# Performance work log

Hardware: AMD Instinct MI355X
Metric: run time of the kernel (lower is better)

## Reference

```python
import jax, jax.numpy as jnp
import numpy as np

N = 4096   # support size
B = 512    # number of histograms (columns)


def setup_inputs() -> dict:
    key = jax.random.key(0)
    kU, kP, kK = jax.random.split(key, 3)
    # u must satisfy u < lamda; uniform [0,1) with lamda=10 is safe.
    U = jax.random.uniform(kU, (N, B), dtype=jnp.float32)
    # strictly positive histograms (avoid log(0))
    P = jax.random.uniform(kP, (N, B), dtype=jnp.float32) + 0.01
    # positive Gibbs kernel
    K = jax.random.uniform(kK, (N, N), dtype=jnp.float32) + 1e-3
    return {"U": U, "P": P, "K": K, "eps": 1, "lamda": 10}


def reference(U, P, K, eps, lamda):
    """Vectorized OTModel.OT_unbal: sum over columns of the primal unbalanced OT
    value reconstructed from dual potential U.  gamma_ij = a_i * K_ij * f_j is
    never materialized; all reductions over gamma are contracted analytically.
    """
    eps = jnp.float32(eps)
    lamda = jnp.float32(lamda)
    # f in log domain: (lamda/eps) * log(lamda/(lamda-u))          [N, B]
    flog = (lamda / eps) * jnp.log(lamda / (lamda - U))
    f = jnp.exp(flog)
    # alpha/eps with the mean-scale stabilization from get_alpha_unbal
    scale = flog.mean(axis=0)                                      # [B]
    KF_stab = K @ jnp.exp(flog - scale)                            # [N, B]
    alpha_over_eps = jnp.log(P) - (jnp.log(KF_stab) + scale)       # [N, B]
    a = jnp.exp(alpha_over_eps)                                    # exp(alpha/eps)
    Kf = K @ f                                                     # [N, B]
    # (gamma @ flog).sum() = sum_i a_i * (K @ (f * flog))_i
    term1 = jnp.sum(a * (K @ (f * flog)))
    # (gamma.T @ (alpha/eps)).sum() = sum_i a_i * (alpha/eps)_i * (K @ f)_i
    term2 = jnp.sum(a * alpha_over_eps * Kf)
    # gamma.sum()
    term3 = jnp.sum(a * Kf)
    # gamma.sum(0)_j = f_j * (K^T @ a)_j
    gcol = f * (K.T @ a)                                           # [N, B]
    # q from get_q_unbal (unstabilized, as in the original)
    q = (lamda / (lamda - U)) ** (lamda / eps + 1.0) * (K.T @ (P / Kf))
    # KL(a,b) = sum(a*log(a/b) - a)   (inputs strictly positive here)
    kl = jnp.sum(gcol * jnp.log(gcol / q) - gcol)
    return eps * (term1 + term2 - term3) + lamda * kl
```

## Files before the change

kernel.cpp:

```cpp
#include <hip/hip_runtime.h>

#define NN 4096
#define BB 512

typedef __attribute__((ext_vector_type(4))) float f32x4;
typedef __attribute__((ext_vector_type(16))) float f32x16;
typedef __attribute__((ext_vector_type(4))) int i32x4;
typedef __attribute__((ext_vector_type(8))) int i32x8;
typedef unsigned short ushort;
typedef unsigned char uchar;
typedef unsigned int uint;
typedef __attribute__((ext_vector_type(4))) ushort ushort4v;

#define ASCALE 16384.0f
#define AINV   6.103515625e-05f
#define SCL1   0x7f7f7f7f

__device__ __forceinline__ float scal_val(const void* p) {
    int b = *(const int*)p;
    if (b >= 1 && b <= 1000000) return (float)b;
    return __int_as_float(b);
}

__device__ __forceinline__ ushort f2bf(float x) {
    unsigned u = __float_as_uint(x);
    u += 0x7fffu + ((u >> 16) & 1u);
    return (ushort)(u >> 16);
}
__device__ __forceinline__ float bf2f(ushort b) {
    return __uint_as_float((uint)b << 16);
}

__device__ __forceinline__ uint pack4_fp8(float a, float b, float c, float d) {
    int v = __builtin_amdgcn_cvt_pk_fp8_f32(a, b, 0, false);
    v = __builtin_amdgcn_cvt_pk_fp8_f32(c, d, v, true);
    return (uint)v;
}

__device__ __forceinline__ void gload16(const void* g, void* l) {
    __builtin_amdgcn_global_load_lds(
        (const __attribute__((address_space(1))) unsigned int*)g,
        (__attribute__((address_space(3))) unsigned int*)l, 16, 0, 0);
}

__device__ __forceinline__ double wave_sum(double v) {
#pragma unroll
    for (int s = 32; s > 0; s >>= 1) v += __shfl_down(v, s, 64);
    return v;
}

__device__ __forceinline__ int offA(int i, int k) {
    return (((i >> 7) * 64 + (k >> 6)) << 13) + ((i & 127) << 6) +
           ((((k >> 4) & 3) ^ ((i >> 1) & 3)) << 4) + (k & 15);
}
__device__ __forceinline__ int offB(int j, int k) {
    return (((j >> 6) * 64 + (k >> 6)) << 12) + ((j & 63) << 6) +
           ((((k >> 4) & 3) ^ ((j >> 1) & 3)) << 4) + (k & 15);
}

__device__ __forceinline__ i32x8 frag64(const uchar* rowbase, int u0byte) {
    i32x4 lo = *(const i32x4*)(rowbase + u0byte);
    i32x4 hi = *(const i32x4*)(rowbase + (u0byte ^ 16));
    i32x8 r;
    r[0] = lo[0]; r[1] = lo[1]; r[2] = lo[2]; r[3] = lo[3];
    r[4] = hi[0]; r[5] = hi[1]; r[6] = hi[2]; r[7] = hi[3];
    return r;
}


__global__ __launch_bounds__(256) void k_prep(const float* __restrict__ K,
                                              const float* __restrict__ U,
                                              uchar* __restrict__ Kb,
                                              uchar* __restrict__ KTb,
                                              uchar* __restrict__ fT,
                                              const void* epsp, const void* lamp) {
    __shared__ float tile[64][65];
    const int t = threadIdx.x;
    const int tx = t & 15, ty = t >> 4;
    const int bid = blockIdx.x;

    if (bid < 4096) {
        const int c0 = (bid & 63) * 64, r0 = (bid >> 6) * 64;
#pragma unroll
        for (int it = 0; it < 4; ++it) {
            int row = ty + it * 16;
            int i = r0 + row;
            float4 v = *(const float4*)&K[(size_t)i * NN + c0 + tx * 4];
            *(uint*)&Kb[offA(i, c0 + tx * 4)] = pack4_fp8(v.x, v.y, v.z, v.w);
            tile[row][tx * 4 + 0] = v.x;
            tile[row][tx * 4 + 1] = v.y;
            tile[row][tx * 4 + 2] = v.z;
            tile[row][tx * 4 + 3] = v.w;
        }
        __syncthreads();
#pragma unroll
        for (int it = 0; it < 4; ++it) {
            int row = ty + it * 16;
            int i = c0 + row;
            int k = r0 + tx * 4;
            *(uint*)&KTb[offA(i, k)] =
                pack4_fp8(tile[tx * 4 + 0][row], tile[tx * 4 + 1][row],
                          tile[tx * 4 + 2][row], tile[tx * 4 + 3][row]);
        }
    } else {
        const int r = bid - 4096;
        const int c0 = (r & 7) * 64;
        const int r0 = (r >> 3) * 64;
        const float eps = scal_val(epsp), lam = scal_val(lamp);
        const float rr = lam / eps;
#pragma unroll
        for (int it = 0; it < 4; ++it) {
            int row = ty + it * 16;
            float4 v = *(const float4*)&U[(size_t)(r0 + row) * BB + c0 + tx * 4];
            float uu[4] = {v.x, v.y, v.z, v.w};
#pragma unroll
            for (int k = 0; k < 4; ++k) {
                float L = __logf(lam / (lam - uu[k]));
                tile[row][tx * 4 + k] = __expf(rr * L);
            }
        }
        __syncthreads();
#pragma unroll
        for (int it = 0; it < 4; ++it) {
            int row = ty + it * 16;
            int j = c0 + row;
            int k = r0 + tx * 4;
            *(uint*)&fT[offB(j, k)] =
                pack4_fp8(tile[tx * 4 + 0][row], tile[tx * 4 + 1][row],
                          tile[tx * 4 + 2][row], tile[tx * 4 + 3][row]);
        }
    }
}

__global__ __launch_bounds__(256) void k_gemm1(const uchar* __restrict__ Kb,
                                               const uchar* __restrict__ fT,
                                               ushort* __restrict__ Y1b) {
    __shared__ __align__(16) uchar As[2][128 * 64];
    __shared__ __align__(16) uchar Bf[2][64 * 64];

    const int tid = threadIdx.x;
    const int lane = tid & 63;
    const int w = tid >> 6;
    const int bid = blockIdx.x;
    const int kh = bid & 3;
    const int i0 = ((bid >> 2) & 31) * 128;
    const int j0 = (bid >> 7) * 64;
    const int h = lane >> 5;
    const int r = lane & 31;
    const int u0b = (((h << 1) ^ ((r >> 1) & 3)) << 4);

    f32x16 acc0 = {}, acc1 = {};

    const uchar* apanel = Kb + ((size_t)(i0 >> 7) << 19);
    const uchar* bpanel = fT + ((size_t)(j0 >> 6) << 18);

    auto stage = [&](int ks, int b) {
        const uchar* ga = apanel + ((size_t)ks << 13) + w * 2048 + lane * 16;
        gload16(ga, &As[b][w * 2048]);
        gload16(ga + 1024, &As[b][w * 2048 + 1024]);
        const uchar* gb = bpanel + ((size_t)ks << 12) + w * 1024 + lane * 16;
        gload16(gb, &Bf[b][w * 1024]);
    };

    const int ks0 = kh * 16;
    stage(ks0, 0);
    __syncthreads();
    for (int step = 0; step < 16; ++step) {
        const int cur = step & 1;
        if (step < 15) stage(ks0 + step + 1, cur ^ 1);
        i32x8 av = frag64(&As[cur][(w * 32 + r) << 6], u0b);
        i32x8 bv0 = frag64(&Bf[cur][r << 6], u0b);
        i32x8 bv1 = frag64(&Bf[cur][(32 + r) << 6], u0b);
        acc0 = __builtin_amdgcn_mfma_scale_f32_32x32x64_f8f6f4(
            av, bv0, acc0, 0, 0, 0, SCL1, 0, SCL1);
        acc1 = __builtin_amdgcn_mfma_scale_f32_32x32x64_f8f6f4(
            av, bv1, acc1, 0, 0, 0, SCL1, 0, SCL1);
        __syncthreads();
    }

    ushort* o1 = Y1b + (size_t)kh * NN * BB;
#pragma unroll
    for (int reg = 0; reg < 16; ++reg) {
        const int row = i0 + w * 32 + (reg & 3) + 8 * (reg >> 2) + 4 * h;
        o1[(size_t)row * BB + j0 + r] = f2bf(acc0[reg]);
        o1[(size_t)row * BB + j0 + 32 + r] = f2bf(acc1[reg]);
    }
}

__global__ __launch_bounds__(256) void k_epi(const ushort* __restrict__ Y1b,
                                             const float* __restrict__ P,
                                             uchar* __restrict__ aT,
                                             double* __restrict__ parts) {
    __shared__ float ta[64][65];
    __shared__ double bred[4][2];
    const int t = threadIdx.x;
    const int lane = t & 63;
    const int w = t >> 6;
    const int tx = t & 15, ty = t >> 4;
    const int j0 = blockIdx.x * 64;
    const int i0 = blockIdx.y * 64;
    const int bid = blockIdx.y * 8 + blockIdx.x;
    const size_t H = (size_t)NN * BB;

    double t2 = 0.0, t3 = 0.0;
#pragma unroll
    for (int it = 0; it < 4; ++it) {
        int row = ty + it * 16;
        size_t off = (size_t)(i0 + row) * BB + j0 + tx * 4;
        ushort4v q0 = *(const ushort4v*)(Y1b + off);
        ushort4v q1 = *(const ushort4v*)(Y1b + H + off);
        ushort4v q2 = *(const ushort4v*)(Y1b + 2 * H + off);
        ushort4v q3 = *(const ushort4v*)(Y1b + 3 * H + off);
        float4 p4 = *(const float4*)(P + off);
        float pv[4] = {p4.x, p4.y, p4.z, p4.w};
#pragma unroll
        for (int e = 0; e < 4; ++e) {
            float y1 = bf2f(q0[e]) + bf2f(q1[e]) + bf2f(q2[e]) + bf2f(q3[e]);
            float aij = pv[e] / y1;
            t2 += (double)(pv[e] * __logf(aij));
            t3 += (double)pv[e];
            ta[row][tx * 4 + e] = aij * ASCALE;
        }
    }
    __syncthreads();
#pragma unroll
    for (int it = 0; it < 4; ++it) {
        int row = ty + it * 16;
        int j = j0 + row;
        *(uint*)&aT[offB(j, i0 + tx * 4)] =
            pack4_fp8(ta[tx * 4 + 0][row], ta[tx * 4 + 1][row],
                      ta[tx * 4 + 2][row], ta[tx * 4 + 3][row]);
    }

    t2 = wave_sum(t2); t3 = wave_sum(t3);
    if (lane == 0) { bred[w][0] = t2; bred[w][1] = t3; }
    __syncthreads();
    if (t == 0) {
        double b = 0, c = 0;
#pragma unroll
        for (int ww = 0; ww < 4; ++ww) { b += bred[ww][0]; c += bred[ww][1]; }
        parts[2048 + bid] = b;
        parts[2560 + bid] = c;
    }
}

__global__ __launch_bounds__(256) void k_gemm2(const uchar* __restrict__ KTb,
                                               const uchar* __restrict__ aT,
                                               const float* __restrict__ U,
                                               const void* epsp, const void* lamp,
                                               double* __restrict__ parts) {
    __shared__ __align__(16) uchar As[2][128 * 64];
    __shared__ __align__(16) uchar Bs[2][64 * 64];
    __shared__ double bred[4][2];

    const float eps = scal_val(epsp), lam = scal_val(lamp);
    const float rr = lam / eps;
    const int tid = threadIdx.x;
    const int lane = tid & 63;
    const int w = tid >> 6;
    const int bid = blockIdx.x;
    const int kh = bid & 3;
    const int i0 = ((bid >> 2) & 31) * 128;
    const int j0 = (bid >> 7) * 64;
    const int h = lane >> 5;
    const int r = lane & 31;
    const int u0b = (((h << 1) ^ ((r >> 1) & 3)) << 4);

    f32x16 acc0 = {}, acc1 = {};

    const uchar* apanel = KTb + ((size_t)(i0 >> 7) << 19);
    const uchar* bpanel = aT + ((size_t)(j0 >> 6) << 18);

    auto stage = [&](int ks, int b) {
        const uchar* ga = apanel + ((size_t)ks << 13) + w * 2048 + lane * 16;
        gload16(ga, &As[b][w * 2048]);
        gload16(ga + 1024, &As[b][w * 2048 + 1024]);
        const uchar* gb = bpanel + ((size_t)ks << 12) + w * 1024 + lane * 16;
        gload16(gb, &Bs[b][w * 1024]);
    };

    const int ks0 = kh * 16;
    stage(ks0, 0);
    __syncthreads();
    for (int step = 0; step < 16; ++step) {
        const int cur = step & 1;
        if (step < 15) stage(ks0 + step + 1, cur ^ 1);
        i32x8 av = frag64(&As[cur][(w * 32 + r) << 6], u0b);
        i32x8 bv0 = frag64(&Bs[cur][r << 6], u0b);
        i32x8 bv1 = frag64(&Bs[cur][(32 + r) << 6], u0b);
        acc0 = __builtin_amdgcn_mfma_scale_f32_32x32x64_f8f6f4(
            av, bv0, acc0, 0, 0, 0, SCL1, 0, SCL1);
        acc1 = __builtin_amdgcn_mfma_scale_f32_32x32x64_f8f6f4(
            av, bv1, acc1, 0, 0, 0, SCL1, 0, SCL1);
        __syncthreads();
    }

    double t1p = 0.0, klp = 0.0;
#pragma unroll
    for (int reg = 0; reg < 16; ++reg) {
        const int ib = i0 + w * 32 + (reg & 3) + 8 * (reg >> 2) + 4 * h;
#pragma unroll
        for (int nt = 0; nt < 2; ++nt) {
            const int j = j0 + nt * 32 + r;
            float s = (nt ? acc1[reg] : acc0[reg]) * AINV;
            float u = U[(size_t)ib * BB + j];
            float L = __logf(lam / (lam - u));
            float fv = __expf(rr * L);
            t1p += (double)(fv * rr * L * s);
            klp -= (double)(fv * (1.0f + L) * s);
        }
    }

    t1p = wave_sum(t1p); klp = wave_sum(klp);
    if (lane == 0) { bred[w][0] = t1p; bred[w][1] = klp; }
    __syncthreads();
    if (tid == 0) {
        double a = 0, b = 0;
#pragma unroll
        for (int ww = 0; ww < 4; ++ww) { a += bred[ww][0]; b += bred[ww][1]; }
        parts[bid] = a;
        parts[1024 + bid] = b;
    }
}

__global__ __launch_bounds__(256) void k_final(const double* __restrict__ parts,
                                               const void* epsp, const void* lamp,
                                               float* __restrict__ out) {
    __shared__ double red[4][4];
    const int tid = threadIdx.x;
    const int lane = tid & 63, w = tid >> 6;
    double s0 = 0.0, s1 = 0.0, s2 = 0.0, s3 = 0.0;
    for (int i = tid; i < 1024; i += 256) {
        s0 += parts[i];
        s1 += parts[1024 + i];
    }
    for (int i = tid; i < 512; i += 256) {
        s2 += parts[2048 + i];
        s3 += parts[2560 + i];
    }
    s0 = wave_sum(s0); s1 = wave_sum(s1); s2 = wave_sum(s2); s3 = wave_sum(s3);
    if (lane == 0) { red[w][0] = s0; red[w][1] = s1; red[w][2] = s2; red[w][3] = s3; }
    __syncthreads();
    if (tid == 0) {
        double t1 = 0, kl = 0, t2 = 0, t3 = 0;
#pragma unroll
        for (int ww = 0; ww < 4; ++ww) {
            t1 += red[ww][0]; kl += red[ww][1]; t2 += red[ww][2]; t3 += red[ww][3];
        }
        float eps = scal_val(epsp), lam = scal_val(lamp);
        out[0] = (float)((double)eps * (t1 + t2 - t3) + (double)lam * kl);
    }
}

extern "C" void kernel_launch(void* const* d_in, const int* in_sizes, int n_in,
                              void* d_out, int out_size, void* d_ws, size_t ws_size,
                              hipStream_t stream) {
    const float* U = (const float*)d_in[0];
    const float* P = (const float*)d_in[1];
    const float* K = (const float*)d_in[2];
    const void* epsp = d_in[3];
    const void* lamp = d_in[4];

    double* parts = (double*)d_ws;
    char* base = (char*)d_ws + (64 << 10);
    uchar* Kb   = (uchar*)base;
    uchar* KTb  = (uchar*)(base + ((size_t)16 << 20));
    uchar* fT   = (uchar*)(base + ((size_t)32 << 20));
    uchar* aT   = (uchar*)(base + ((size_t)34 << 20));
    ushort* Y1b = (ushort*)(base + ((size_t)36 << 20));

    k_prep<<<4608, 256, 0, stream>>>(K, U, Kb, KTb, fT, epsp, lamp);
    k_gemm1<<<1024, 256, 0, stream>>>(Kb, fT, Y1b);
    k_epi<<<dim3(8, 64), 256, 0, stream>>>(Y1b, P, aT, parts);
    k_gemm2<<<1024, 256, 0, stream>>>(KTb, aT, U, epsp, lamp, parts);
    k_final<<<1, 256, 0, stream>>>(parts, epsp, lamp, (float*)d_out);
}
```

Before: 156.0 us.

## Enlarge GEMM block tile to 128x128 with 2x2 wave grid and 8-way split-K

Both FP8 GEMM kernels now compute a 128x128 output tile per block. Each wave owns a 64x64 sub-tile (2x2 MFMAs), so every loaded A and B fragment is reused twice. To keep the block count the same, split-K doubles from 4 to 8 slices, and each block runs 8 K-steps instead of 16. Launch bounds now request 4 blocks per CU. The price is that the epilogue must read and sum 8 bf16 partial planes of Y1 instead of 4, and the intermediate buffer must hold twice as many planes.

Result: slower. 179.1 us (+14.8%).

```diff
diff --git a/kernel.cpp b/kernel.cpp
--- a/kernel.cpp
+++ b/kernel.cpp
@@ -132,24 +132,29 @@
     }
 }
 
-__global__ __launch_bounds__(256) void k_gemm1(const uchar* __restrict__ Kb,
-                                               const uchar* __restrict__ fT,
-                                               ushort* __restrict__ Y1b) {
+__global__ __launch_bounds__(256, 4) void k_gemm1(const uchar* __restrict__ Kb,
+                                                  const uchar* __restrict__ fT,
+                                                  ushort* __restrict__ Y1b) {
     __shared__ __align__(16) uchar As[2][128 * 64];
-    __shared__ __align__(16) uchar Bf[2][64 * 64];
+    __shared__ __align__(16) uchar Bs[2][128 * 64];
 
     const int tid = threadIdx.x;
     const int lane = tid & 63;
     const int w = tid >> 6;
+    const int wm = w >> 1, wn = w & 1;
     const int bid = blockIdx.x;
-    const int kh = bid & 3;
-    const int i0 = ((bid >> 2) & 31) * 128;
-    const int j0 = (bid >> 7) * 64;
+    const int kh = bid & 7;
+    const int i0 = ((bid >> 3) & 31) * 128;
+    const int j0 = (bid >> 8) * 128;
     const int h = lane >> 5;
     const int r = lane & 31;
     const int u0b = (((h << 1) ^ ((r >> 1) & 3)) << 4);
 
-    f32x16 acc0 = {}, acc1 = {};
+    f32x16 acc[2][2];
+#pragma unroll
+    for (int mt = 0; mt < 2; ++mt)
+#pragma unroll
+        for (int nt = 0; nt < 2; ++nt) acc[mt][nt] = (f32x16)(0.0f);
 
     const uchar* apanel = Kb + ((size_t)(i0 >> 7) << 19);
     const uchar* bpanel = fT + ((size_t)(j0 >> 6) << 18);
@@ -158,33 +163,47 @@
         const uchar* ga = apanel + ((size_t)ks << 13) + w * 2048 + lane * 16;
         gload16(ga, &As[b][w * 2048]);
         gload16(ga + 1024, &As[b][w * 2048 + 1024]);
-        const uchar* gb = bpanel + ((size_t)ks << 12) + w * 1024 + lane * 16;
-        gload16(gb, &Bf[b][w * 1024]);
+        const uchar* gb = bpanel + (((size_t)(w >> 1)) << 18) +
+                          ((size_t)ks << 12) + (w & 1) * 2048 + lane * 16;
+        gload16(gb, &Bs[b][w * 2048]);
+        gload16(gb + 1024, &Bs[b][w * 2048 + 1024]);
     };
 
-    const int ks0 = kh * 16;
+    const int ks0 = kh * 8;
     stage(ks0, 0);
     __syncthreads();
-    for (int step = 0; step < 16; ++step) {
+    for (int step = 0; step < 8; ++step) {
         const int cur = step & 1;
-        if (step < 15) stage(ks0 + step + 1, cur ^ 1);
-        i32x8 av = frag64(&As[cur][(w * 32 + r) << 6], u0b);
-        i32x8 bv0 = frag64(&Bf[cur][r << 6], u0b);
-        i32x8 bv1 = frag64(&Bf[cur][(32 + r) << 6], u0b);
-        acc0 = __builtin_amdgcn_mfma_scale_f32_32x32x64_f8f6f4(
-            av, bv0, acc0, 0, 0, 0, SCL1, 0, SCL1);
-        acc1 = __builtin_amdgcn_mfma_scale_f32_32x32x64_f8f6f4(
-            av, bv1, acc1, 0, 0, 0, SCL1, 0, SCL1);
+        if (step < 7) stage(ks0 + step + 1, cur ^ 1);
+        i32x8 av[2], bv[2];
+#pragma unroll
+        for (int mt = 0; mt < 2; ++mt)
+            av[mt] = frag64(&As[cur][(wm * 64 + mt * 32 + r) << 6], u0b);
+#pragma unroll
+        for (int nt = 0; nt < 2; ++nt)
+            bv[nt] = frag64(&Bs[cur][(wn * 64 + nt * 32 + r) << 6], u0b);
+#pragma unroll
+        for (int mt = 0; mt < 2; ++mt)
+#pragma unroll
+            for (int nt = 0; nt < 2; ++nt)
+                acc[mt][nt] = __builtin_amdgcn_mfma_scale_f32_32x32x64_f8f6f4(
+                    av[mt], bv[nt], acc[mt][nt], 0, 0, 0, SCL1, 0, SCL1);
         __syncthreads();
     }
 
     ushort* o1 = Y1b + (size_t)kh * NN * BB;
 #pragma unroll
-    for (int reg = 0; reg < 16; ++reg) {
-        const int row = i0 + w * 32 + (reg & 3) + 8 * (reg >> 2) + 4 * h;
-        o1[(size_t)row * BB + j0 + r] = f2bf(acc0[reg]);
-        o1[(size_t)row * BB + j0 + 32 + r] = f2bf(acc1[reg]);
-    }
+    for (int mt = 0; mt < 2; ++mt)
+#pragma unroll
+        for (int nt = 0; nt < 2; ++nt) {
+            const int jb = j0 + wn * 64 + nt * 32 + r;
+#pragma unroll
+            for (int reg = 0; reg < 16; ++reg) {
+                const int row =
+                    i0 + wm * 64 + mt * 32 + (reg & 3) + 8 * (reg >> 2) + 4 * h;
+                o1[(size_t)row * BB + jb] = f2bf(acc[mt][nt][reg]);
+            }
+        }
 }
 
 __global__ __launch_bounds__(256) void k_epi(const ushort* __restrict__ Y1b,
@@ -207,16 +226,18 @@
     for (int it = 0; it < 4; ++it) {
         int row = ty + it * 16;
         size_t off = (size_t)(i0 + row) * BB + j0 + tx * 4;
-        ushort4v q0 = *(const ushort4v*)(Y1b + off);
-        ushort4v q1 = *(const ushort4v*)(Y1b + H + off);
-        ushort4v q2 = *(const ushort4v*)(Y1b + 2 * H + off);
-        ushort4v q3 = *(const ushort4v*)(Y1b + 3 * H + off);
+        float y1[4] = {0.f, 0.f, 0.f, 0.f};
+#pragma unroll
+        for (int pl = 0; pl < 8; ++pl) {
+            ushort4v qq = *(const ushort4v*)(Y1b + (size_t)pl * H + off);
+#pragma unroll
+            for (int e = 0; e < 4; ++e) y1[e] += bf2f(qq[e]);
+        }
         float4 p4 = *(const float4*)(P + off);
         float pv[4] = {p4.x, p4.y, p4.z, p4.w};
 #pragma unroll
         for (int e = 0; e < 4; ++e) {
-            float y1 = bf2f(q0[e]) + bf2f(q1[e]) + bf2f(q2[e]) + bf2f(q3[e]);
-            float aij = pv[e] / y1;
+            float aij = pv[e] / y1[e];
             t2 += (double)(pv[e] * __logf(aij));
             t3 += (double)pv[e];
             ta[row][tx * 4 + e] = aij * ASCALE;
@@ -244,13 +265,13 @@
     }
 }
 
-__global__ __launch_bounds__(256) void k_gemm2(const uchar* __restrict__ KTb,
-                                               const uchar* __restrict__ aT,
-                                               const float* __restrict__ U,
-                                               const void* epsp, const void* lamp,
-                                               double* __restrict__ parts) {
+__global__ __launch_bounds__(256, 4) void k_gemm2(const uchar* __restrict__ KTb,
+                                                  const uchar* __restrict__ aT,
+                                                  const float* __restrict__ U,
+                                                  const void* epsp, const void* lamp,
+                                                  double* __restrict__ parts) {
     __shared__ __align__(16) uchar As[2][128 * 64];
-    __shared__ __align__(16) uchar Bs[2][64 * 64];
+    __shared__ __align__(16) uchar Bs[2][128 * 64];
     __shared__ double bred[4][2];
 
     const float eps = scal_val(epsp), lam = scal_val(lamp);
@@ -258,15 +279,20 @@
     const int tid = threadIdx.x;
     const int lane = tid & 63;
     const int w = tid >> 6;
+    const int wm = w >> 1, wn = w & 1;
     const int bid = blockIdx.x;
-    const int kh = bid & 3;
-    const int i0 = ((bid >> 2) & 31) * 128;
-    const int j0 = (bid >> 7) * 64;
+    const int kh = bid & 7;
+    const int i0 = ((bid >> 3) & 31) * 128;
+    const int j0 = (bid >> 8) * 128;
     const int h = lane >> 5;
     const int r = lane & 31;
     const int u0b = (((h << 1) ^ ((r >> 1) & 3)) << 4);
 
-    f32x16 acc0 = {}, acc1 = {};
+    f32x16 acc[2][2];
+#pragma unroll
+    for (int mt = 0; mt < 2; ++mt)
+#pragma unroll
+        for (int nt = 0; nt < 2; ++nt) acc[mt][nt] = (f32x16)(0.0f);
 
     const uchar* apanel = KTb + ((size_t)(i0 >> 7) << 19);
     const uchar* bpanel = aT + ((size_t)(j0 >> 6) << 18);
@@ -275,41 +301,52 @@
         const uchar* ga = apanel + ((size_t)ks << 13) + w * 2048 + lane * 16;
         gload16(ga, &As[b][w * 2048]);
         gload16(ga + 1024, &As[b][w * 2048 + 1024]);
-        const uchar* gb = bpanel + ((size_t)ks << 12) + w * 1024 + lane * 16;
-        gload16(gb, &Bs[b][w * 1024]);
+        const uchar* gb = bpanel + (((size_t)(w >> 1)) << 18) +
+                          ((size_t)ks << 12) + (w & 1) * 2048 + lane * 16;
+        gload16(gb, &Bs[b][w * 2048]);
+        gload16(gb + 1024, &Bs[b][w * 2048 + 1024]);
     };
 
-    const int ks0 = kh * 16;
+    const int ks0 = kh * 8;
     stage(ks0, 0);
     __syncthreads();
-    for (int step = 0; step < 16; ++step) {
+    for (int step = 0; step < 8; ++step) {
         const int cur = step & 1;
-        if (step < 15) stage(ks0 + step + 1, cur ^ 1);
-        i32x8 av = frag64(&As[cur][(w * 32 + r) << 6], u0b);
-        i32x8 bv0 = frag64(&Bs[cur][r << 6], u0b);
-        i32x8 bv1 = frag64(&Bs[cur][(32 + r) << 6], u0b);
-        acc0 = __builtin_amdgcn_mfma_scale_f32_32x32x64_f8f6f4(
-            av, bv0, acc0, 0, 0, 0, SCL1, 0, SCL1);
-        acc1 = __builtin_amdgcn_mfma_scale_f32_32x32x64_f8f6f4(
-            av, bv1, acc1, 0, 0, 0, SCL1, 0, SCL1);
+        if (step < 7) stage(ks0 + step + 1, cur ^ 1);
+        i32x8 av[2], bv[2];
+#pragma unroll
+        for (int mt = 0; mt < 2; ++mt)
+            av[mt] = frag64(&As[cur][(wm * 64 + mt * 32 + r) << 6], u0b);
+#pragma unroll
+        for (int nt = 0; nt < 2; ++nt)
+            bv[nt] = frag64(&Bs[cur][(wn * 64 + nt * 32 + r) << 6], u0b);
+#pragma unroll
+        for (int mt = 0; mt < 2; ++mt)
+#pragma unroll
+            for (int nt = 0; nt < 2; ++nt)
+                acc[mt][nt] = __builtin_amdgcn_mfma_scale_f32_32x32x64_f8f6f4(
+                    av[mt], bv[nt], acc[mt][nt], 0, 0, 0, SCL1, 0, SCL1);
         __syncthreads();
     }
 
     double t1p = 0.0, klp = 0.0;
 #pragma unroll
-    for (int reg = 0; reg < 16; ++reg) {
-        const int ib = i0 + w * 32 + (reg & 3) + 8 * (reg >> 2) + 4 * h;
+    for (int mt = 0; mt < 2; ++mt)
 #pragma unroll
         for (int nt = 0; nt < 2; ++nt) {
-            const int j = j0 + nt * 32 + r;
-            float s = (nt ? acc1[reg] : acc0[reg]) * AINV;
-            float u = U[(size_t)ib * BB + j];
-            float L = __logf(lam / (lam - u));
-            float fv = __expf(rr * L);
-            t1p += (double)(fv * rr * L * s);
-            klp -= (double)(fv * (1.0f + L) * s);
-        }
-    }
+            const int jb = j0 + wn * 64 + nt * 32 + r;
+#pragma unroll
+            for (int reg = 0; reg < 16; ++reg) {
+                const int ib =
+                    i0 + wm * 64 + mt * 32 + (reg & 3) + 8 * (reg >> 2) + 4 * h;
+                float s = acc[mt][nt][reg] * AINV;
+                float u = U[(size_t)ib * BB + jb];
+                float L = __logf(lam / (lam - u));
+                float fv = __expf(rr * L);
+                t1p += (double)(fv * rr * L * s);
+                klp -= (double)(fv * (1.0f + L) * s);
+            }
+        }
 
     t1p = wave_sum(t1p); klp = wave_sum(klp);
     if (lane == 0) { bred[w][0] = t1p; bred[w][1] = klp; }
```

## Double K-tile per stage in fp8 GEMMs and fold final reduction into gemm2

Applied to the files above, without the earlier changes.

Both fp8 MFMA GEMM kernels now stage 128 bytes of K per pipeline step instead of 64, halving the number of loop iterations and __syncthreads barriers, at the cost of double the LDS footprint (which may lower occupancy). The separate single-block final-reduction kernel is removed: gemm2 blocks increment an atomic counter (zeroed in k_prep), and the last block to finish sums the partial results and writes the output. This saves one kernel launch, at the cost of a threadfence and an atomic per block.

Measured after the change: 192.1 us. 23.1% more time.

```diff
diff --git a/kernel.cpp b/kernel.cpp
--- a/kernel.cpp
+++ b/kernel.cpp
@@ -73,11 +73,14 @@
                                               uchar* __restrict__ Kb,
                                               uchar* __restrict__ KTb,
                                               uchar* __restrict__ fT,
-                                              const void* epsp, const void* lamp) {
+                                              const void* epsp, const void* lamp,
+                                              double* __restrict__ parts) {
     __shared__ float tile[64][65];
     const int t = threadIdx.x;
     const int tx = t & 15, ty = t >> 4;
     const int bid = blockIdx.x;
+
+    if (bid == 0 && t == 0) *(unsigned int*)(parts + 3072) = 0u;
 
     if (bid < 4096) {
         const int c0 = (bid & 63) * 64, r0 = (bid >> 6) * 64;
@@ -135,8 +138,8 @@
 __global__ __launch_bounds__(256) void k_gemm1(const uchar* __restrict__ Kb,
                                                const uchar* __restrict__ fT,
                                                ushort* __restrict__ Y1b) {
-    __shared__ __align__(16) uchar As[2][128 * 64];
-    __shared__ __align__(16) uchar Bf[2][64 * 64];
+    __shared__ __align__(16) uchar As[2][128 * 128];
+    __shared__ __align__(16) uchar Bf[2][64 * 128];
 
     const int tid = threadIdx.x;
     const int lane = tid & 63;
@@ -154,27 +157,35 @@
     const uchar* apanel = Kb + ((size_t)(i0 >> 7) << 19);
     const uchar* bpanel = fT + ((size_t)(j0 >> 6) << 18);
 
-    auto stage = [&](int ks, int b) {
-        const uchar* ga = apanel + ((size_t)ks << 13) + w * 2048 + lane * 16;
-        gload16(ga, &As[b][w * 2048]);
-        gload16(ga + 1024, &As[b][w * 2048 + 1024]);
-        const uchar* gb = bpanel + ((size_t)ks << 12) + w * 1024 + lane * 16;
-        gload16(gb, &Bf[b][w * 1024]);
+    auto stage = [&](int step, int b) {
+        const int ks = (kh * 16) + step * 2;
+        const uchar* ga = apanel + ((size_t)ks << 13) + w * 4096 + lane * 16;
+        gload16(ga, &As[b][w * 4096]);
+        gload16(ga + 1024, &As[b][w * 4096 + 1024]);
+        gload16(ga + 2048, &As[b][w * 4096 + 2048]);
+        gload16(ga + 3072, &As[b][w * 4096 + 3072]);
+        const uchar* gb = bpanel + ((size_t)ks << 12) + w * 2048 + lane * 16;
+        gload16(gb, &Bf[b][w * 2048]);
+        gload16(gb + 1024, &Bf[b][w * 2048 + 1024]);
     };
 
-    const int ks0 = kh * 16;
-    stage(ks0, 0);
-    __syncthreads();
-    for (int step = 0; step < 16; ++step) {
+    stage(0, 0);
+    __syncthreads();
+    for (int step = 0; step < 8; ++step) {
         const int cur = step & 1;
-        if (step < 15) stage(ks0 + step + 1, cur ^ 1);
-        i32x8 av = frag64(&As[cur][(w * 32 + r) << 6], u0b);
-        i32x8 bv0 = frag64(&Bf[cur][r << 6], u0b);
-        i32x8 bv1 = frag64(&Bf[cur][(32 + r) << 6], u0b);
-        acc0 = __builtin_amdgcn_mfma_scale_f32_32x32x64_f8f6f4(
-            av, bv0, acc0, 0, 0, 0, SCL1, 0, SCL1);
-        acc1 = __builtin_amdgcn_mfma_scale_f32_32x32x64_f8f6f4(
-            av, bv1, acc1, 0, 0, 0, SCL1, 0, SCL1);
+        if (step < 7) stage(step + 1, cur ^ 1);
+#pragma unroll
+        for (int kk = 0; kk < 2; ++kk) {
+            const uchar* abase = &As[cur][kk * 8192];
+            const uchar* bbase = &Bf[cur][kk * 4096];
+            i32x8 av = frag64(abase + ((w * 32 + r) << 6), u0b);
+            i32x8 bv0 = frag64(bbase + (r << 6), u0b);
+            i32x8 bv1 = frag64(bbase + ((32 + r) << 6), u0b);
+            acc0 = __builtin_amdgcn_mfma_scale_f32_32x32x64_f8f6f4(
+                av, bv0, acc0, 0, 0, 0, SCL1, 0, SCL1);
+            acc1 = __builtin_amdgcn_mfma_scale_f32_32x32x64_f8f6f4(
+                av, bv1, acc1, 0, 0, 0, SCL1, 0, SCL1);
+        }
         __syncthreads();
     }
 
@@ -248,10 +259,12 @@
                                                const uchar* __restrict__ aT,
                                                const float* __restrict__ U,
                                                const void* epsp, const void* lamp,
-                                               double* __restrict__ parts) {
-    __shared__ __align__(16) uchar As[2][128 * 64];
-    __shared__ __align__(16) uchar Bs[2][64 * 64];
-    __shared__ double bred[4][2];
+                                               double* __restrict__ parts,
+                                               float* __restrict__ out) {
+    __shared__ __align__(16) uchar As[2][128 * 128];
+    __shared__ __align__(16) uchar Bs[2][64 * 128];
+    __shared__ double bred[4][4];
+    __shared__ int lastflag;
 
     const float eps = scal_val(epsp), lam = scal_val(lamp);
     const float rr = lam / eps;
@@ -271,27 +284,35 @@
     const uchar* apanel = KTb + ((size_t)(i0 >> 7) << 19);
     const uchar* bpanel = aT + ((size_t)(j0 >> 6) << 18);
 
-    auto stage = [&](int ks, int b) {
-        const uchar* ga = apanel + ((size_t)ks << 13) + w * 2048 + lane * 16;
-        gload16(ga, &As[b][w * 2048]);
-        gload16(ga + 1024, &As[b][w * 2048 + 1024]);
-        const uchar* gb = bpanel + ((size_t)ks << 12) + w * 1024 + lane * 16;
-        gload16(gb, &Bs[b][w * 1024]);
+    auto stage = [&](int step, int b) {
+        const int ks = (kh * 16) + step * 2;
+        const uchar* ga = apanel + ((size_t)ks << 13) + w * 4096 + lane * 16;
+        gload16(ga, &As[b][w * 4096]);
+        gload16(ga + 1024, &As[b][w * 4096 + 1024]);
+        gload16(ga + 2048, &As[b][w * 4096 + 2048]);
+        gload16(ga + 3072, &As[b][w * 4096 + 3072]);
+        const uchar* gb = bpanel + ((size_t)ks << 12) + w * 2048 + lane * 16;
+        gload16(gb, &Bs[b][w * 2048]);
+        gload16(gb + 1024, &Bs[b][w * 2048 + 1024]);
     };
 
-    const int ks0 = kh * 16;
-    stage(ks0, 0);
-    __syncthreads();
-    for (int step = 0; step < 16; ++step) {
+    stage(0, 0);
+    __syncthreads();
+    for (int step = 0; step < 8; ++step) {
         const int cur = step & 1;
-        if (step < 15) stage(ks0 + step + 1, cur ^ 1);
-        i32x8 av = frag64(&As[cur][(w * 32 + r) << 6], u0b);
-        i32x8 bv0 = frag64(&Bs[cur][r << 6], u0b);
-        i32x8 bv1 = frag64(&Bs[cur][(32 + r) << 6], u0b);
-        acc0 = __builtin_amdgcn_mfma_scale_f32_32x32x64_f8f6f4(
-            av, bv0, acc0, 0, 0, 0, SCL1, 0, SCL1);
-        acc1 = __builtin_amdgcn_mfma_scale_f32_32x32x64_f8f6f4(
-            av, bv1, acc1, 0, 0, 0, SCL1, 0, SCL1);
+        if (step < 7) stage(step + 1, cur ^ 1);
+#pragma unroll
+        for (int kk = 0; kk < 2; ++kk) {
+            const uchar* abase = &As[cur][kk * 8192];
+            const uchar* bbase = &Bs[cur][kk * 4096];
+            i32x8 av = frag64(abase + ((w * 32 + r) << 6), u0b);
+            i32x8 bv0 = frag64(bbase + (r << 6), u0b);
+            i32x8 bv1 = frag64(bbase + ((32 + r) << 6), u0b);
+            acc0 = __builtin_amdgcn_mfma_scale_f32_32x32x64_f8f6f4(
+                av, bv0, acc0, 0, 0, 0, SCL1, 0, SCL1);
+            acc1 = __builtin_amdgcn_mfma_scale_f32_32x32x64_f8f6f4(
+                av, bv1, acc1, 0, 0, 0, SCL1, 0, SCL1);
+        }
         __syncthreads();
     }
 
@@ -320,35 +341,39 @@
         for (int ww = 0; ww < 4; ++ww) { a += bred[ww][0]; b += bred[ww][1]; }
         parts[bid] = a;
         parts[1024 + bid] = b;
-    }
-}
-
-__global__ __launch_bounds__(256) void k_final(const double* __restrict__ parts,
-                                               const void* epsp, const void* lamp,
-                                               float* __restrict__ out) {
-    __shared__ double red[4][4];
-    const int tid = threadIdx.x;
-    const int lane = tid & 63, w = tid >> 6;
-    double s0 = 0.0, s1 = 0.0, s2 = 0.0, s3 = 0.0;
-    for (int i = tid; i < 1024; i += 256) {
-        s0 += parts[i];
-        s1 += parts[1024 + i];
-    }
-    for (int i = tid; i < 512; i += 256) {
-        s2 += parts[2048 + i];
-        s3 += parts[2560 + i];
-    }
-    s0 = wave_sum(s0); s1 = wave_sum(s1); s2 = wave_sum(s2); s3 = wave_sum(s3);
-    if (lane == 0) { red[w][0] = s0; red[w][1] = s1; red[w][2] = s2; red[w][3] = s3; }
-    __syncthreads();
-    if (tid == 0) {
-        double t1 = 0, kl = 0, t2 = 0, t3 = 0;
-#pragma unroll
-        for (int ww = 0; ww < 4; ++ww) {
-            t1 += red[ww][0]; kl += red[ww][1]; t2 += red[ww][2]; t3 += red[ww][3];
-        }
-        float eps = scal_val(epsp), lam = scal_val(lamp);
-        out[0] = (float)((double)eps * (t1 + t2 - t3) + (double)lam * kl);
+        __threadfence();
+        uint old = atomicAdd((unsigned int*)(parts + 3072), 1u);
+        lastflag = (old == 1023) ? 1 : 0;
+    }
+    __syncthreads();
+
+    if (lastflag) {
+        __threadfence();
+        const volatile double* vp = parts;
+        double s0 = 0.0, s1 = 0.0, s2 = 0.0, s3 = 0.0;
+        for (int i = tid; i < 1024; i += 256) {
+            s0 += vp[i];
+            s1 += vp[1024 + i];
+        }
+        for (int i = tid; i < 512; i += 256) {
+            s2 += vp[2048 + i];
+            s3 += vp[2560 + i];
+        }
+        s0 = wave_sum(s0); s1 = wave_sum(s1);
+        s2 = wave_sum(s2); s3 = wave_sum(s3);
+        if (lane == 0) {
+            bred[w][0] = s0; bred[w][1] = s1; bred[w][2] = s2; bred[w][3] = s3;
+        }
+        __syncthreads();
+        if (tid == 0) {
+            double t1 = 0, kl = 0, t2 = 0, t3 = 0;
+#pragma unroll
+            for (int ww = 0; ww < 4; ++ww) {
+                t1 += bred[ww][0]; kl += bred[ww][1];
+                t2 += bred[ww][2]; t3 += bred[ww][3];
+            }
+            out[0] = (float)((double)eps * (t1 + t2 - t3) + (double)lam * kl);
+        }
     }
 }
 
@@ -369,9 +394,8 @@
     uchar* aT   = (uchar*)(base + ((size_t)34 << 20));
     ushort* Y1b = (ushort*)(base + ((size_t)36 << 20));
 
-    k_prep<<<4608, 256, 0, stream>>>(K, U, Kb, KTb, fT, epsp, lamp);
+    k_prep<<<4608, 256, 0, stream>>>(K, U, Kb, KTb, fT, epsp, lamp, parts);
     k_gemm1<<<1024, 256, 0, stream>>>(Kb, fT, Y1b);
     k_epi<<<dim3(8, 64), 256, 0, stream>>>(Y1b, P, aT, parts);
-    k_gemm2<<<1024, 256, 0, stream>>>(KTb, aT, U, epsp, lamp, parts);
-    k_final<<<1, 256, 0, stream>>>(parts, epsp, lamp, (float*)d_out);
-}
+    k_gemm2<<<1024, 256, 0, stream>>>(KTb, aT, U, epsp, lamp, parts, (float*)d_out);
+}
```

## Widen GEMM tiles to 128x128 with 8 waves and register-staged double buffering

Applied to the files above, without the earlier changes.

Both FP8 GEMM kernels now use 512-thread blocks that each compute a 128x128 output tile, split across a 4x2 wave grid, so the grid shrinks from 1024 to 512 blocks. This halves the re-reads of each K panel. The direct global-to-LDS loads are replaced by prefetching tiles into registers two steps ahead and then writing them to LDS. The intent is better operand reuse and more latency hiding, at the cost of fewer blocks in flight, extra register pressure and explicit LDS store instructions. k_final now reads only 512 partials per term to match the new grid.

Result: no change. 157.7 us (+1.1%).

```diff
diff --git a/kernel.cpp b/kernel.cpp
--- a/kernel.cpp
+++ b/kernel.cpp
@@ -35,12 +35,6 @@
     int v = __builtin_amdgcn_cvt_pk_fp8_f32(a, b, 0, false);
     v = __builtin_amdgcn_cvt_pk_fp8_f32(c, d, v, true);
     return (uint)v;
-}
-
-__device__ __forceinline__ void gload16(const void* g, void* l) {
-    __builtin_amdgcn_global_load_lds(
-        (const __attribute__((address_space(1))) unsigned int*)g,
-        (__attribute__((address_space(3))) unsigned int*)l, 16, 0, 0);
 }
 
 __device__ __forceinline__ double wave_sum(double v) {
@@ -132,19 +126,20 @@
     }
 }
 
-__global__ __launch_bounds__(256) void k_gemm1(const uchar* __restrict__ Kb,
+__global__ __launch_bounds__(512) void k_gemm1(const uchar* __restrict__ Kb,
                                                const uchar* __restrict__ fT,
                                                ushort* __restrict__ Y1b) {
     __shared__ __align__(16) uchar As[2][128 * 64];
-    __shared__ __align__(16) uchar Bf[2][64 * 64];
+    __shared__ __align__(16) uchar Bs[2][2 * 64 * 64];
 
     const int tid = threadIdx.x;
     const int lane = tid & 63;
     const int w = tid >> 6;
+    const int wm = w >> 1, wn = w & 1;
     const int bid = blockIdx.x;
     const int kh = bid & 3;
     const int i0 = ((bid >> 2) & 31) * 128;
-    const int j0 = (bid >> 7) * 64;
+    const int j0 = (bid >> 7) * 128;
     const int h = lane >> 5;
     const int r = lane & 31;
     const int u0b = (((h << 1) ^ ((r >> 1) & 3)) << 4);
@@ -154,36 +149,46 @@
     const uchar* apanel = Kb + ((size_t)(i0 >> 7) << 19);
     const uchar* bpanel = fT + ((size_t)(j0 >> 6) << 18);
 
-    auto stage = [&](int ks, int b) {
-        const uchar* ga = apanel + ((size_t)ks << 13) + w * 2048 + lane * 16;
-        gload16(ga, &As[b][w * 2048]);
-        gload16(ga + 1024, &As[b][w * 2048 + 1024]);
-        const uchar* gb = bpanel + ((size_t)ks << 12) + w * 1024 + lane * 16;
-        gload16(gb, &Bf[b][w * 1024]);
+    i32x4 ra, rb;
+    auto ldregs = [&](int ks) {
+        ra = *(const i32x4*)(apanel + ((size_t)ks << 13) + w * 1024 + lane * 16);
+        rb = *(const i32x4*)(bpanel + ((size_t)(w >> 2) << 18) +
+                             ((size_t)ks << 12) + (w & 3) * 1024 + lane * 16);
     };
+    auto wrlds = [&](int b) {
+        *(i32x4*)&As[b][w * 1024 + lane * 16] = ra;
+        *(i32x4*)&Bs[b][w * 1024 + lane * 16] = rb;
+    };
 
     const int ks0 = kh * 16;
-    stage(ks0, 0);
-    __syncthreads();
+    ldregs(ks0);
+    wrlds(0);
+    ldregs(ks0 + 1);
+    __syncthreads();
+    int cur = 0;
     for (int step = 0; step < 16; ++step) {
-        const int cur = step & 1;
-        if (step < 15) stage(ks0 + step + 1, cur ^ 1);
-        i32x8 av = frag64(&As[cur][(w * 32 + r) << 6], u0b);
-        i32x8 bv0 = frag64(&Bf[cur][r << 6], u0b);
-        i32x8 bv1 = frag64(&Bf[cur][(32 + r) << 6], u0b);
+        if (step < 15) {
+            wrlds(cur ^ 1);
+            if (step < 14) ldregs(ks0 + step + 2);
+        }
+        i32x8 av = frag64(&As[cur][(wm * 32 + r) << 6], u0b);
+        i32x8 bv0 = frag64(&Bs[cur][(wn * 64 + r) << 6], u0b);
+        i32x8 bv1 = frag64(&Bs[cur][(wn * 64 + 32 + r) << 6], u0b);
         acc0 = __builtin_amdgcn_mfma_scale_f32_32x32x64_f8f6f4(
             av, bv0, acc0, 0, 0, 0, SCL1, 0, SCL1);
         acc1 = __builtin_amdgcn_mfma_scale_f32_32x32x64_f8f6f4(
             av, bv1, acc1, 0, 0, 0, SCL1, 0, SCL1);
         __syncthreads();
+        cur ^= 1;
     }
 
     ushort* o1 = Y1b + (size_t)kh * NN * BB;
+    const int jb = j0 + wn * 64 + r;
 #pragma unroll
     for (int reg = 0; reg < 16; ++reg) {
-        const int row = i0 + w * 32 + (reg & 3) + 8 * (reg >> 2) + 4 * h;
-        o1[(size_t)row * BB + j0 + r] = f2bf(acc0[reg]);
-        o1[(size_t)row * BB + j0 + 32 + r] = f2bf(acc1[reg]);
+        const int row = i0 + wm * 32 + (reg & 3) + 8 * (reg >> 2) + 4 * h;
+        o1[(size_t)row * BB + jb] = f2bf(acc0[reg]);
+        o1[(size_t)row * BB + jb + 32] = f2bf(acc1[reg]);
     }
 }
 
@@ -244,24 +249,25 @@
     }
 }
 
-__global__ __launch_bounds__(256) void k_gemm2(const uchar* __restrict__ KTb,
+__global__ __launch_bounds__(512) void k_gemm2(const uchar* __restrict__ KTb,
                                                const uchar* __restrict__ aT,
                                                const float* __restrict__ U,
                                                const void* epsp, const void* lamp,
                                                double* __restrict__ parts) {
     __shared__ __align__(16) uchar As[2][128 * 64];
-    __shared__ __align__(16) uchar Bs[2][64 * 64];
-    __shared__ double bred[4][2];
+    __shared__ __align__(16) uchar Bs[2][2 * 64 * 64];
+    __shared__ double bred[8][2];
 
     const float eps = scal_val(epsp), lam = scal_val(lamp);
     const float rr = lam / eps;
     const int tid = threadIdx.x;
     const int lane = tid & 63;
     const int w = tid >> 6;
+    const int wm = w >> 1, wn = w & 1;
     const int bid = blockIdx.x;
     const int kh = bid & 3;
     const int i0 = ((bid >> 2) & 31) * 128;
-    const int j0 = (bid >> 7) * 64;
+    const int j0 = (bid >> 7) * 128;
     const int h = lane >> 5;
     const int r = lane & 31;
     const int u0b = (((h << 1) ^ ((r >> 1) & 3)) << 4);
@@ -271,37 +277,47 @@
     const uchar* apanel = KTb + ((size_t)(i0 >> 7) << 19);
     const uchar* bpanel = aT + ((size_t)(j0 >> 6) << 18);
 
-    auto stage = [&](int ks, int b) {
-        const uchar* ga = apanel + ((size_t)ks << 13) + w * 2048 + lane * 16;
-        gload16(ga, &As[b][w * 2048]);
-        gload16(ga + 1024, &As[b][w * 2048 + 1024]);
-        const uchar* gb = bpanel + ((size_t)ks << 12) + w * 1024 + lane * 16;
-        gload16(gb, &Bs[b][w * 1024]);
+    i32x4 ra, rb;
+    auto ldregs = [&](int ks) {
+        ra = *(const i32x4*)(apanel + ((size_t)ks << 13) + w * 1024 + lane * 16);
+        rb = *(const i32x4*)(bpanel + ((size_t)(w >> 2) << 18) +
+                             ((size_t)ks << 12) + (w & 3) * 1024 + lane * 16);
     };
+    auto wrlds = [&](int b) {
+        *(i32x4*)&As[b][w * 1024 + lane * 16] = ra;
+        *(i32x4*)&Bs[b][w * 1024 + lane * 16] = rb;
+    };
 
     const int ks0 = kh * 16;
-    stage(ks0, 0);
-    __syncthreads();
+    ldregs(ks0);
+    wrlds(0);
+    ldregs(ks0 + 1);
+    __syncthreads();
+    int cur = 0;
     for (int step = 0; step < 16; ++step) {
-        const int cur = step & 1;
-        if (step < 15) stage(ks0 + step + 1, cur ^ 1);
-        i32x8 av = frag64(&As[cur][(w * 32 + r) << 6], u0b);
-        i32x8 bv0 = frag64(&Bs[cur][r << 6], u0b);
-        i32x8 bv1 = frag64(&Bs[cur][(32 + r) << 6], u0b);
+        if (step < 15) {
+            wrlds(cur ^ 1);
+            if (step < 14) ldregs(ks0 + step + 2);
+        }
+        i32x8 av = frag64(&As[cur][(wm * 32 + r) << 6], u0b);
+        i32x8 bv0 = frag64(&Bs[cur][(wn * 64 + r) << 6], u0b);
+        i32x8 bv1 = frag64(&Bs[cur][(wn * 64 + 32 + r) << 6], u0b);
         acc0 = __builtin_amdgcn_mfma_scale_f32_32x32x64_f8f6f4(
             av, bv0, acc0, 0, 0, 0, SCL1, 0, SCL1);
         acc1 = __builtin_amdgcn_mfma_scale_f32_32x32x64_f8f6f4(
             av, bv1, acc1, 0, 0, 0, SCL1, 0, SCL1);
         __syncthreads();
+        cur ^= 1;
     }
 
     double t1p = 0.0, klp = 0.0;
+    const int jb = j0 + wn * 64 + r;
 #pragma unroll
     for (int reg = 0; reg < 16; ++reg) {
-        const int ib = i0 + w * 32 + (reg & 3) + 8 * (reg >> 2) + 4 * h;
+        const int ib = i0 + wm * 32 + (reg & 3) + 8 * (reg >> 2) + 4 * h;
 #pragma unroll
         for (int nt = 0; nt < 2; ++nt) {
-            const int j = j0 + nt * 32 + r;
+            const int j = jb + nt * 32;
             float s = (nt ? acc1[reg] : acc0[reg]) * AINV;
             float u = U[(size_t)ib * BB + j];
             float L = __logf(lam / (lam - u));
@@ -317,7 +333,7 @@
     if (tid == 0) {
         double a = 0, b = 0;
 #pragma unroll
-        for (int ww = 0; ww < 4; ++ww) { a += bred[ww][0]; b += bred[ww][1]; }
+        for (int ww = 0; ww < 8; ++ww) { a += bred[ww][0]; b += bred[ww][1]; }
         parts[bid] = a;
         parts[1024 + bid] = b;
     }
@@ -330,11 +346,9 @@
     const int tid = threadIdx.x;
     const int lane = tid & 63, w = tid >> 6;
     double s0 = 0.0, s1 = 0.0, s2 = 0.0, s3 = 0.0;
-    for (int i = tid; i < 1024; i += 256) {
+    for (int i = tid; i < 512; i += 256) {
         s0 += parts[i];
         s1 += parts[1024 + i];
-    }
-    for (int i = tid; i < 512; i += 256) {
         s2 += parts[2048 + i];
         s3 += parts[2560 + i];
     }
@@ -370,8 +384,8 @@
     ushort* Y1b = (ushort*)(base + ((size_t)36 << 20));
 
     k_prep<<<4608, 256, 0, stream>>>(K, U, Kb, KTb, fT, epsp, lamp);
-    k_gemm1<<<1024, 256, 0, stream>>>(Kb, fT, Y1b);
+    k_gemm1<<<512, 512, 0, stream>>>(Kb, fT, Y1b);
     k_epi<<<dim3(8, 64), 256, 0, stream>>>(Y1b, P, aT, parts);
-    k_gemm2<<<1024, 256, 0, stream>>>(KTb, aT, U, epsp, lamp, parts);
+    k_gemm2<<<512, 512, 0, stream>>>(KTb, aT, U, epsp, lamp, parts);
     k_final<<<1, 256, 0, stream>>>(parts, epsp, lamp, (float*)d_out);
 }
```
